# Kernel optimization log

Measured on AMD Instinct MI355X. Metric: run time of the kernel, lower is better.

The kernel has to match this reference:

```python
import jax, jax.numpy as jnp
import numpy as np

N, E, D, B, C = 50000, 800000, 128, 20000, 40
EPS_BN = 1e-3    # keras BatchNormalization default epsilon
EPS_NRM = 1e-12  # keras ops.nn.normalize epsilon
FFN_DIMS = {"pre": (D, D), "c1p": (D, D), "c1u": (2 * D, D), "c2p": (D, D), "c2u": (2 * D, D), "post": (D, D)}


def setup_inputs() -> dict:
    key = jax.random.key(0)
    ks = jax.random.split(key, 8)
    inp = {
        "node_features": jax.random.normal(ks[0], (N, D), jnp.float32),
        "edges": jax.random.randint(ks[1], (2, E), 0, N, dtype=jnp.int32),
        "edge_w": jax.random.uniform(ks[2], (E,), jnp.float32),
        "input_node_idx": jax.random.randint(ks[3], (B,), 0, N, dtype=jnp.int32),
    }
    for i, (name, (din, dout)) in enumerate(FFN_DIMS.items()):
        kw = jax.random.fold_in(key, 100 + i)
        inp[name + "_g"] = jnp.ones((din,), jnp.float32)
        inp[name + "_be"] = jnp.zeros((din,), jnp.float32)
        inp[name + "_mu"] = jnp.zeros((din,), jnp.float32)
        inp[name + "_var"] = jnp.ones((din,), jnp.float32)
        inp[name + "_w"] = jax.random.normal(kw, (din, dout), jnp.float32) * (1.0 / float(np.sqrt(din)))
        inp[name + "_bi"] = jnp.zeros((dout,), jnp.float32)
    inp["logits_w"] = jax.random.normal(ks[4], (D, C), jnp.float32) * (1.0 / float(np.sqrt(D)))
    inp["logits_b"] = jnp.zeros((C,), jnp.float32)
    return inp


def ffn(x, g, be, mu, var, w, bi):
    # BatchNorm (inference running stats) -> Dropout (identity) -> Dense + exact gelu
    xn = (x - mu) * jax.lax.rsqrt(var + EPS_BN) * g + be
    return jax.nn.gelu(xn @ w + bi, approximate=False)


def l2norm(x):
    n = jnp.sqrt(jnp.sum(x * x, axis=-1, keepdims=True))
    return x / jnp.maximum(n, EPS_NRM)


def graph_conv(x, node_idx, nbr_idx, ew, prep, upd):
    # gather neighbours -> prepare FFN -> edge-weighted -> segment_sum (reduce='sum')
    msgs = ffn(x[nbr_idx], *prep) * ew[:, None]                         # [E, D]
    red = jax.ops.segment_sum(msgs, node_idx, num_segments=x.shape[0])  # [N, D]
    h = jnp.concatenate([x, red], axis=1)                               # [N, 2D] (combination='concat')
    return l2norm(ffn(h, *upd))                                         # normalize=True


def reference(node_features, edges, edge_w, input_node_idx,
              pre_g, pre_be, pre_mu, pre_var, pre_w, pre_bi,
              c1p_g, c1p_be, c1p_mu, c1p_var, c1p_w, c1p_bi,
              c1u_g, c1u_be, c1u_mu, c1u_var, c1u_w, c1u_bi,
              c2p_g, c2p_be, c2p_mu, c2p_var, c2p_w, c2p_bi,
              c2u_g, c2u_be, c2u_mu, c2u_var, c2u_w, c2u_bi,
              post_g, post_be, post_mu, post_var, post_w, post_bi,
              logits_w, logits_b):
    ew = edge_w / jnp.sum(edge_w)                       # edge_W normalized at init
    node_idx, nbr_idx = edges[0], edges[1]
    x = ffn(node_features, pre_g, pre_be, pre_mu, pre_var, pre_w, pre_bi)
    x = graph_conv(x, node_idx, nbr_idx, ew,
                   (c1p_g, c1p_be, c1p_mu, c1p_var, c1p_w, c1p_bi),
                   (c1u_g, c1u_be, c1u_mu, c1u_var, c1u_w, c1u_bi)) + x
    x = graph_conv(x, node_idx, nbr_idx, ew,
                   (c2p_g, c2p_be, c2p_mu, c2p_var, c2p_w, c2p_bi),
                   (c2u_g, c2u_be, c2u_mu, c2u_var, c2u_w, c2u_bi)) + x
    x = ffn(x, post_g, post_be, post_mu, post_var, post_w, post_bi)
    return x[input_node_idx] @ logits_w + logits_b      # [B, C]
```

## Files before the change

kernel.cpp:

```cpp
#include <hip/hip_runtime.h>
#include <hip/hip_fp16.h>
#include <math.h>

static constexpr int D = 128;
static constexpr int CAP = 64;
static constexpr float EPS_BN = 1e-3f;

typedef short short8 __attribute__((ext_vector_type(8)));
typedef short short4v __attribute__((ext_vector_type(4)));
typedef float float4v __attribute__((ext_vector_type(4)));

__device__ __forceinline__ float gelu_exact(float x) {
    return 0.5f * x * (1.0f + erff(x * 0.70710678118654752f));
}

__device__ __forceinline__ void f32_to_hilo(float f, short& h, short& l) {
    unsigned u = __float_as_uint(f);
    h = (short)(u >> 16);
    float hf = __uint_as_float(u & 0xFFFF0000u);
    unsigned lu = __float_as_uint(f - hf);
    l = (short)(lu >> 16);
}

__device__ __forceinline__ short f32_to_bf16_rne(float f) {
    unsigned u = __float_as_uint(f);
    u += 0x7FFFu + ((u >> 16) & 1u);
    return (short)(u >> 16);
}

__device__ __forceinline__ void cvt_hilo8(const float4& x, const float4& y, short8& h8, short8& l8) {
    short h, l;
    f32_to_hilo(x.x, h, l); h8[0] = h; l8[0] = l;
    f32_to_hilo(x.y, h, l); h8[1] = h; l8[1] = l;
    f32_to_hilo(x.z, h, l); h8[2] = h; l8[2] = l;
    f32_to_hilo(x.w, h, l); h8[3] = h; l8[3] = l;
    f32_to_hilo(y.x, h, l); h8[4] = h; l8[4] = l;
    f32_to_hilo(y.y, h, l); h8[5] = h; l8[5] = l;
    f32_to_hilo(y.z, h, l); h8[6] = h; l8[6] = l;
    f32_to_hilo(y.w, h, l); h8[7] = h; l8[7] = l;
}

__device__ __forceinline__ short8 cvt_rne8(const float4& x, const float4& y) {
    short8 r;
    r[0] = f32_to_bf16_rne(x.x); r[1] = f32_to_bf16_rne(x.y);
    r[2] = f32_to_bf16_rne(x.z); r[3] = f32_to_bf16_rne(x.w);
    r[4] = f32_to_bf16_rne(y.x); r[5] = f32_to_bf16_rne(y.y);
    r[6] = f32_to_bf16_rne(y.z); r[7] = f32_to_bf16_rne(y.w);
    return r;
}

struct FoldArgs {
    const float* g[6]; const float* be[6]; const float* mu[6];
    const float* var[6]; const float* w[6]; const float* bi[6];
    short* wh[6]; short* wl[6]; float* bp[6]; int K[6];
};

__global__ void k_fold(FoldArgs fa) {
    __shared__ float sm[4];
    const int tid = threadIdx.x;
    const int lane = tid & 63, wvi = tid >> 6;
    const int f = blockIdx.x >> 7;
    const int c = blockIdx.x & 127;
    const int K = fa.K[f];
    const float* g = fa.g[f]; const float* be = fa.be[f];
    const float* mu = fa.mu[f]; const float* var = fa.var[f];
    const float* w = fa.w[f]; const float* bi = fa.bi[f];
    short* wh = fa.wh[f]; short* wl = fa.wl[f]; float* bp = fa.bp[f];
    float part = 0.f;
    for (int k = tid; k < K; k += blockDim.x) {
        float a = g[k] / sqrtf(var[k] + EPS_BN);
        float wv = w[k * D + c];
        float prod = a * wv;
        short hh, ll;
        f32_to_hilo(prod, hh, ll);
        wh[c * K + k] = hh;
        wl[c * K + k] = ll;
        part += (be[k] - mu[k] * a) * wv;
    }
    for (int off = 32; off > 0; off >>= 1) part += __shfl_down(part, off, 64);
    if (lane == 0) sm[wvi] = part;
    __syncthreads();
    if (tid == 0) bp[c] = bi[c] + sm[0] + sm[1] + sm[2] + sm[3];
}

__global__ void __launch_bounds__(512, 4) k_fillpre(
    const int* __restrict__ edges, const float* __restrict__ ew,
    int* __restrict__ cnt, float* __restrict__ sums, unsigned* __restrict__ cw,
    int E, int N,
    const float* __restrict__ A0, const short* __restrict__ Wh,
    const short* __restrict__ Wl, const float* __restrict__ bp,
    float* __restrict__ outf,
    const short* __restrict__ Wh1, const float* __restrict__ bp1,
    __half* __restrict__ yh)
{
    constexpr int K = 128;
    constexpr int WSZ = 128 * K;
    __shared__ short Wlds[2 * WSZ];
    __shared__ short xbuf[2][16][136];
    __shared__ float sm[8];

    const int tid = threadIdx.x;
    const int lane = tid & 63;
    const int wvi = tid >> 6;

    const int grp = blockIdx.x >> 8;
    const int role = grp & 1;
    const int rid = ((grp >> 1) << 8) | (blockIdx.x & 255);

    if (role == 0) {
        const int g = rid & 7;
        const int bid = rid >> 3;
        const int gs = 64 * 512;
        const int N8 = (N + 7) >> 3;
        const int lo = g * N8;
        const int hi = min(lo + N8, N);
        float s = 0.f;
        int e = bid * 512 + tid;
        for (; e + 3 * gs < E; e += 4 * gs) {
            int d0 = edges[e];
            int d1 = edges[e + gs];
            int d2 = edges[e + 2 * gs];
            int d3 = edges[e + 3 * gs];
            bool i0 = (d0 >= lo && d0 < hi);
            bool i1 = (d1 >= lo && d1 < hi);
            bool i2 = (d2 >= lo && d2 < hi);
            bool i3 = (d3 >= lo && d3 < hi);
            int s0 = 0, s1 = 0, s2 = 0, s3 = 0;
            float w0 = 0.f, w1 = 0.f, w2 = 0.f, w3 = 0.f;
            if (i0) { s0 = edges[E + e];          w0 = ew[e]; }
            if (i1) { s1 = edges[E + e + gs];     w1 = ew[e + gs]; }
            if (i2) { s2 = edges[E + e + 2 * gs]; w2 = ew[e + 2 * gs]; }
            if (i3) { s3 = edges[E + e + 3 * gs]; w3 = ew[e + 3 * gs]; }
            if (i0) { s += w0; int x = atomicAdd(&cnt[d0], 1);
                if (x < CAP) cw[(size_t)d0 * CAP + x] = ((unsigned)s0 << 16) | (unsigned)__half_as_ushort(__float2half(w0)); }
            if (i1) { s += w1; int x = atomicAdd(&cnt[d1], 1);
                if (x < CAP) cw[(size_t)d1 * CAP + x] = ((unsigned)s1 << 16) | (unsigned)__half_as_ushort(__float2half(w1)); }
            if (i2) { s += w2; int x = atomicAdd(&cnt[d2], 1);
                if (x < CAP) cw[(size_t)d2 * CAP + x] = ((unsigned)s2 << 16) | (unsigned)__half_as_ushort(__float2half(w2)); }
            if (i3) { s += w3; int x = atomicAdd(&cnt[d3], 1);
                if (x < CAP) cw[(size_t)d3 * CAP + x] = ((unsigned)s3 << 16) | (unsigned)__half_as_ushort(__float2half(w3)); }
        }
        for (; e < E; e += gs) {
            int d = edges[e];
            if (d >= lo && d < hi) {
                int src = edges[E + e];
                float w = ew[e];
                s += w;
                int x = atomicAdd(&cnt[d], 1);
                if (x < CAP)
                    cw[(size_t)d * CAP + x] = ((unsigned)src << 16) | (unsigned)__half_as_ushort(__float2half(w));
            }
        }
        for (int off = 32; off > 0; off >>= 1) s += __shfl_down(s, off, 64);
        if (lane == 0) sm[wvi] = s;
        __syncthreads();
        if (tid == 0) {
            float t = 0.f;
            #pragma unroll
            for (int i = 0; i < 8; i++) t += sm[i];
            if (t != 0.f) atomicAdd(sums, t);
        }
        return;
    }

    const int fbid = rid;
    constexpr int NBLK = 512;

    #pragma unroll
    for (int it = 0; it < (2 * WSZ) / (512 * 8); ++it) {
        int s = it * 4096 + tid * 8;
        int buf = s / WSZ;
        int rem = s - buf * WSZ;
        int c = rem / K;
        int kk = (rem & (K - 1)) ^ ((c & 7) << 3);
        const short* src = (buf ? Wl : Wh) + c * K + kk;
        *(short8*)&Wlds[s] = *(const short8*)src;
    }
    __syncthreads();

    const int wv = tid >> 6;
    const int ssub = wv >> 2;
    const int wc = wv & 3;
    const int m = lane & 15;
    const int quad = lane >> 4;
    const int nstrips = (N + 15) >> 4;
    constexpr int STRIDE = NBLK * 2;

    short8 w1f[2][2][2];
    #pragma unroll
    for (int cc = 0; cc < 2; ++cc)
        #pragma unroll
        for (int ks = 0; ks < 2; ++ks)
            #pragma unroll
            for (int tj = 0; tj < 2; ++tj) {
                const int kk = cc * 64 + ks * 32 + quad * 8;
                const int c = wc * 32 + tj * 16 + m;
                w1f[cc][ks][tj] = *(const short8*)(Wh1 + (size_t)c * 128 + kk);
            }

    int remw = nstrips - fbid * 2;
    int nit = remw > 0 ? (remw + STRIDE - 1) / STRIDE : 0;

    for (int it = 0; it < nit; ++it) {
        const int strip = fbid * 2 + ssub + it * STRIDE;
        const bool active = strip < nstrips;
        float4v acc[2];
        acc[0] = (float4v){0.f, 0.f, 0.f, 0.f};
        acc[1] = (float4v){0.f, 0.f, 0.f, 0.f};

        if (active) {
            int r = strip * 16 + m;
            if (r >= N) r = N - 1;
            const float* pA0 = A0 + (size_t)r * D;

            float4 a[2][4];
            {
                const float4* s4 = (const float4*)pA0 + quad * 2;
                a[0][0] = s4[0]; a[0][1] = s4[1]; a[0][2] = s4[8]; a[0][3] = s4[9];
            }
            {
                const float4* s4 = (const float4*)(pA0 + 64) + quad * 2;
                a[1][0] = s4[0]; a[1][1] = s4[1]; a[1][2] = s4[8]; a[1][3] = s4[9];
            }

            #pragma unroll
            for (int cc = 0; cc < 2; ++cc) {
                #pragma unroll
                for (int ks = 0; ks < 2; ++ks) {
                    const int kk = cc * 64 + ks * 32 + quad * 8;
                    short8 ah, al;
                    cvt_hilo8(a[cc][ks * 2], a[cc][ks * 2 + 1], ah, al);
                    #pragma unroll
                    for (int tj = 0; tj < 2; ++tj) {
                        const int c = wc * 32 + tj * 16 + m;
                        const int idx = c * K + (kk ^ ((c & 7) << 3));
                        short8 bh = *(const short8*)&Wlds[idx];
                        short8 bl = *(const short8*)&Wlds[WSZ + idx];
                        acc[tj] = __builtin_amdgcn_mfma_f32_16x16x32_bf16(al, bh, acc[tj], 0, 0, 0);
                        acc[tj] = __builtin_amdgcn_mfma_f32_16x16x32_bf16(ah, bl, acc[tj], 0, 0, 0);
                        acc[tj] = __builtin_amdgcn_mfma_f32_16x16x32_bf16(ah, bh, acc[tj], 0, 0, 0);
                    }
                }
            }

            #pragma unroll
            for (int tj = 0; tj < 2; ++tj) {
                float bv = bp[wc * 32 + tj * 16 + m];
                #pragma unroll
                for (int r4 = 0; r4 < 4; ++r4)
                    acc[tj][r4] = gelu_exact(acc[tj][r4] + bv);
            }
            #pragma unroll
            for (int r4 = 0; r4 < 4; ++r4) {
                int rib = quad * 4 + r4;
                int row = strip * 16 + rib;
                #pragma unroll
                for (int tj = 0; tj < 2; ++tj) {
                    int col = wc * 32 + tj * 16 + m;
                    if (row < N) outf[(size_t)row * D + col] = acc[tj][r4];
                    xbuf[ssub][rib][col] = f32_to_bf16_rne(acc[tj][r4]);
                }
            }
        }
        __syncthreads();

        if (active) {
            float4v acc2[2];
            acc2[0] = (float4v){0.f, 0.f, 0.f, 0.f};
            acc2[1] = (float4v){0.f, 0.f, 0.f, 0.f};
            #pragma unroll
            for (int cc = 0; cc < 2; ++cc) {
                #pragma unroll
                for (int ks = 0; ks < 2; ++ks) {
                    const int kk = cc * 64 + ks * 32 + quad * 8;
                    short8 ah = *(const short8*)&xbuf[ssub][m][kk];
                    #pragma unroll
                    for (int tj = 0; tj < 2; ++tj)
                        acc2[tj] = __builtin_amdgcn_mfma_f32_16x16x32_bf16(ah, w1f[cc][ks][tj], acc2[tj], 0, 0, 0);
                }
            }
            #pragma unroll
            for (int tj = 0; tj < 2; ++tj) {
                float bv = bp1[wc * 32 + tj * 16 + m];
                #pragma unroll
                for (int r4 = 0; r4 < 4; ++r4)
                    acc2[tj][r4] = gelu_exact(acc2[tj][r4] + bv);
            }
            #pragma unroll
            for (int r4 = 0; r4 < 4; ++r4) {
                int row = strip * 16 + quad * 4 + r4;
                if (row < N) {
                    #pragma unroll
                    for (int tj = 0; tj < 2; ++tj) {
                        int col = wc * 32 + tj * 16 + m;
                        yh[(size_t)row * D + col] = __float2half(acc2[tj][r4]);
                    }
                }
            }
        }
        __syncthreads();
    }
}

__device__ __forceinline__ void accum8(float* acc, const float4& raw, float w) {
    const __half2* hp = (const __half2*)&raw;
    #pragma unroll
    for (int t = 0; t < 4; t++) {
        float2 f = __half22float2(hp[t]);
        acc[t * 2]     += w * f.x;
        acc[t * 2 + 1] += w * f.y;
    }
}

__global__ void k_reduce(const int* __restrict__ cnt, const unsigned* __restrict__ cw,
                         const float* __restrict__ sums, const __half* __restrict__ y,
                         float* __restrict__ red, int N) {
    int n = blockIdx.x * (blockDim.x >> 6) + (threadIdx.x >> 6);
    if (n >= N) return;
    float inv = 1.0f / sums[0];
    int lane = threadIdx.x & 63;
    int sub = lane >> 4;
    int q = lane & 15;
    int count = min(cnt[n], CAP);
    int start = n * CAP;
    int end = start + count;
    float acc[8] = {0.f, 0.f, 0.f, 0.f, 0.f, 0.f, 0.f, 0.f};
    int i = start + sub;
    for (; i + 12 < end; i += 16) {
        unsigned c0 = cw[i];
        unsigned c1 = cw[i + 4];
        unsigned c2 = cw[i + 8];
        unsigned c3 = cw[i + 12];
        float4 r0 = *((const float4*)(y + (size_t)(c0 >> 16) * D) + q);
        float4 r1 = *((const float4*)(y + (size_t)(c1 >> 16) * D) + q);
        float4 r2 = *((const float4*)(y + (size_t)(c2 >> 16) * D) + q);
        float4 r3 = *((const float4*)(y + (size_t)(c3 >> 16) * D) + q);
        float w0 = __half2float(__ushort_as_half((unsigned short)(c0 & 0xFFFFu))) * inv;
        float w1 = __half2float(__ushort_as_half((unsigned short)(c1 & 0xFFFFu))) * inv;
        float w2 = __half2float(__ushort_as_half((unsigned short)(c2 & 0xFFFFu))) * inv;
        float w3 = __half2float(__ushort_as_half((unsigned short)(c3 & 0xFFFFu))) * inv;
        accum8(acc, r0, w0);
        accum8(acc, r1, w1);
        accum8(acc, r2, w2);
        accum8(acc, r3, w3);
    }
    for (; i < end; i += 4) {
        unsigned c = cw[i];
        float4 r = *((const float4*)(y + (size_t)(c >> 16) * D) + q);
        float w = __half2float(__ushort_as_half((unsigned short)(c & 0xFFFFu))) * inv;
        accum8(acc, r, w);
    }
    #pragma unroll
    for (int t = 0; t < 8; t++) {
        acc[t] += __shfl_xor(acc[t], 16, 64);
        acc[t] += __shfl_xor(acc[t], 32, 64);
    }
    if (sub == 0) {
        float4 o0 = {acc[0], acc[1], acc[2], acc[3]};
        float4 o1 = {acc[4], acc[5], acc[6], acc[7]};
        *((float4*)(red + (size_t)n * D + q * 8)) = o0;
        *((float4*)(red + (size_t)n * D + q * 8 + 4)) = o1;
    }
}

template<int K, int BLOCK, bool SPLIT3, bool L2RES, bool OUT16, bool GATHER, bool FUSEP>
__global__ void __launch_bounds__(BLOCK, BLOCK / 256) k_ffn(
    const float* __restrict__ A0, const float* __restrict__ A1,
    const short* __restrict__ Wh, const short* __restrict__ Wl,
    const float* __restrict__ bp, const float* __restrict__ resid,
    float* __restrict__ outf, __half* __restrict__ outh, int N,
    const int* __restrict__ gidx,
    const short* __restrict__ WhP, const float* __restrict__ bpP,
    __half* __restrict__ yhP)
{
    constexpr int NB = SPLIT3 ? 2 : 1;
    constexpr int WSZ = 128 * K;
    constexpr int NC = K / 64;
    constexpr int SS = BLOCK / 256;
    __shared__ short Wlds[NB * WSZ];
    __shared__ float rsum[SS][16][4];
    __shared__ short xbuf[FUSEP ? SS : 1][16][136];

    const int tid = threadIdx.x;

    constexpr int ITER = (NB * WSZ) / (BLOCK * 8);
    #pragma unroll
    for (int it = 0; it < ITER; ++it) {
        int s = it * (BLOCK * 8) + tid * 8;
        int buf = s / WSZ;
        int rem = s - buf * WSZ;
        int c = rem / K;
        int kk = (rem & (K - 1)) ^ ((c & 7) << 3);
        const short* src = (buf ? Wl : Wh) + c * K + kk;
        *(short8*)&Wlds[s] = *(const short8*)src;
    }
    __syncthreads();

    const int lane = tid & 63;
    const int wv = tid >> 6;
    const int ssub = wv >> 2;
    const int wc = wv & 3;
    const int m = lane & 15;
    const int quad = lane >> 4;
    const int nstrips = (N + 15) >> 4;
    const int stride = gridDim.x * SS;
    const int base = blockIdx.x * SS + ssub;

    auto body = [&](int strip, bool active) {
        int rr = active ? strip * 16 + m : m;
        if (rr >= N) rr = N - 1;
        const int r = GATHER ? gidx[rr] : rr;
        const float* pA0 = A0 + (size_t)r * D;
        const float* pA1 = (K == 256) ? (A1 + (size_t)r * D) : pA0;

        float4 a[2][4];
        {
            const float4* s4 = (const float4*)pA0 + quad * 2;
            a[0][0] = s4[0]; a[0][1] = s4[1]; a[0][2] = s4[8]; a[0][3] = s4[9];
        }
        {
            const float4* s4 = (const float4*)(pA0 + 64) + quad * 2;
            a[1][0] = s4[0]; a[1][1] = s4[1]; a[1][2] = s4[8]; a[1][3] = s4[9];
        }

        float4v acc[2];
        acc[0] = (float4v){0.f, 0.f, 0.f, 0.f};
        acc[1] = (float4v){0.f, 0.f, 0.f, 0.f};

        #pragma unroll
        for (int cc = 0; cc < NC; ++cc) {
            #pragma unroll
            for (int ks = 0; ks < 2; ++ks) {
                const int kk = cc * 64 + ks * 32 + quad * 8;
                short8 ah, al;
                if (SPLIT3) cvt_hilo8(a[cc & 1][ks * 2], a[cc & 1][ks * 2 + 1], ah, al);
                else        ah = cvt_rne8(a[cc & 1][ks * 2], a[cc & 1][ks * 2 + 1]);
                #pragma unroll
                for (int tj = 0; tj < 2; ++tj) {
                    const int c = wc * 32 + tj * 16 + m;
                    const int idx = c * K + (kk ^ ((c & 7) << 3));
                    short8 bh = *(const short8*)&Wlds[idx];
                    if (SPLIT3) {
                        short8 bl = *(const short8*)&Wlds[WSZ + idx];
                        acc[tj] = __builtin_amdgcn_mfma_f32_16x16x32_bf16(al, bh, acc[tj], 0, 0, 0);
                        acc[tj] = __builtin_amdgcn_mfma_f32_16x16x32_bf16(ah, bl, acc[tj], 0, 0, 0);
                    }
                    acc[tj] = __builtin_amdgcn_mfma_f32_16x16x32_bf16(ah, bh, acc[tj], 0, 0, 0);
                }
            }
            if (cc + 2 < NC) {
                const int n2 = cc + 2;
                const float* src = (K == 256 && n2 >= 2) ? pA1 : pA0;
                const int kb = (K == 256) ? ((n2 & 1) * 64) : (n2 * 64);
                const float4* s4 = (const float4*)(src + kb) + quad * 2;
                a[cc & 1][0] = s4[0]; a[cc & 1][1] = s4[1];
                a[cc & 1][2] = s4[8]; a[cc & 1][3] = s4[9];
            }
        }

        #pragma unroll
        for (int tj = 0; tj < 2; ++tj) {
            float bv = bp[wc * 32 + tj * 16 + m];
            #pragma unroll
            for (int r4 = 0; r4 < 4; ++r4)
                acc[tj][r4] = gelu_exact(acc[tj][r4] + bv);
        }

        if (L2RES) {
            float ss[4];
            #pragma unroll
            for (int r4 = 0; r4 < 4; ++r4) {
                float v = acc[0][r4] * acc[0][r4] + acc[1][r4] * acc[1][r4];
                v += __shfl_xor(v, 1, 64);
                v += __shfl_xor(v, 2, 64);
                v += __shfl_xor(v, 4, 64);
                v += __shfl_xor(v, 8, 64);
                ss[r4] = v;
            }
            if (m == 0) {
                #pragma unroll
                for (int r4 = 0; r4 < 4; ++r4) rsum[ssub][quad * 4 + r4][wc] = ss[r4];
            }
            __syncthreads();
            #pragma unroll
            for (int r4 = 0; r4 < 4; ++r4) {
                const int rib = quad * 4 + r4;
                float tot = rsum[ssub][rib][0] + rsum[ssub][rib][1]
                          + rsum[ssub][rib][2] + rsum[ssub][rib][3];
                float inv = 1.0f / fmaxf(sqrtf(tot), 1e-12f);
                int row = strip * 16 + rib;
                if (active && row < N) {
                    #pragma unroll
                    for (int tj = 0; tj < 2; ++tj) {
                        int col = wc * 32 + tj * 16 + m;
                        float v = acc[tj][r4] * inv + resid[(size_t)row * D + col];
                        outf[(size_t)row * D + col] = v;
                        if (FUSEP) xbuf[ssub][rib][col] = f32_to_bf16_rne(v);
                    }
                }
            }
            if (FUSEP) {
                __syncthreads();
                if (active) {
                    float4v acc2[2];
                    acc2[0] = (float4v){0.f, 0.f, 0.f, 0.f};
                    acc2[1] = (float4v){0.f, 0.f, 0.f, 0.f};
                    #pragma unroll
                    for (int cc = 0; cc < 2; ++cc) {
                        #pragma unroll
                        for (int ks = 0; ks < 2; ++ks) {
                            const int kk = cc * 64 + ks * 32 + quad * 8;
                            short8 ah = *(const short8*)&xbuf[ssub][m][kk];
                            #pragma unroll
                            for (int tj = 0; tj < 2; ++tj) {
                                const int c = wc * 32 + tj * 16 + m;
                                short8 bh = *(const short8*)(WhP + (size_t)c * 128 + kk);
                                acc2[tj] = __builtin_amdgcn_mfma_f32_16x16x32_bf16(ah, bh, acc2[tj], 0, 0, 0);
                            }
                        }
                    }
                    #pragma unroll
                    for (int tj = 0; tj < 2; ++tj) {
                        float bv = bpP[wc * 32 + tj * 16 + m];
                        #pragma unroll
                        for (int r4 = 0; r4 < 4; ++r4)
                            acc2[tj][r4] = gelu_exact(acc2[tj][r4] + bv);
                    }
                    #pragma unroll
                    for (int r4 = 0; r4 < 4; ++r4) {
                        int row = strip * 16 + quad * 4 + r4;
                        if (row < N) {
                            #pragma unroll
                            for (int tj = 0; tj < 2; ++tj) {
                                int col = wc * 32 + tj * 16 + m;
                                yhP[(size_t)row * D + col] = __float2half(acc2[tj][r4]);
                            }
                        }
                    }
                }
            }
            __syncthreads();
        } else {
            #pragma unroll
            for (int r4 = 0; r4 < 4; ++r4) {
                int row = strip * 16 + quad * 4 + r4;
                if (active && row < N) {
                    #pragma unroll
                    for (int tj = 0; tj < 2; ++tj) {
                        int col = wc * 32 + tj * 16 + m;
                        if (OUT16) outh[(size_t)row * D + col] = __float2half(acc[tj][r4]);
                        else       outf[(size_t)row * D + col] = acc[tj][r4];
                    }
                }
            }
        }
    };

    if (L2RES) {
        int rem = nstrips - blockIdx.x * SS;
        int nit = rem > 0 ? (rem + stride - 1) / stride : 0;
        for (int it = 0; it < nit; ++it) {
            int strip = base + it * stride;
            body(strip, strip < nstrips);
        }
    } else {
        for (int strip = base; strip < nstrips; strip += stride)
            body(strip, true);
    }
}

__global__ void k_logits(const float* __restrict__ x,
                         const float* __restrict__ LW, const float* __restrict__ lb,
                         float* __restrict__ out, int B) {
    int wid = blockIdx.x * 4 + (threadIdx.x >> 6);
    int lane = threadIdx.x & 63;
    if (wid >= B) return;
    if (lane >= 40) return;
    float acc = lb[lane];
    const float4* xr = (const float4*)(x + (size_t)wid * D);
    #pragma unroll 4
    for (int k4 = 0; k4 < 32; k4++) {
        float4 xv = xr[k4];
        acc += xv.x * LW[(4 * k4 + 0) * 40 + lane];
        acc += xv.y * LW[(4 * k4 + 1) * 40 + lane];
        acc += xv.z * LW[(4 * k4 + 2) * 40 + lane];
        acc += xv.w * LW[(4 * k4 + 3) * 40 + lane];
    }
    out[(size_t)wid * 40 + lane] = acc;
}

extern "C" void kernel_launch(void* const* d_in, const int* in_sizes, int n_in,
                              void* d_out, int out_size, void* d_ws, size_t ws_size,
                              hipStream_t stream) {
    const float* node_features = (const float*)d_in[0];
    const int*   edges         = (const int*)d_in[1];
    const float* edge_w        = (const float*)d_in[2];
    const int*   input_idx     = (const int*)d_in[3];
    const int N = in_sizes[0] / D;
    const int E = in_sizes[2];
    const int B = in_sizes[3];

    const float* P[6][6];
    for (int f = 0; f < 6; f++)
        for (int q = 0; q < 6; q++)
            P[f][q] = (const float*)d_in[4 + f * 6 + q];
    const float* logits_w = (const float*)d_in[40];
    const float* logits_b = (const float*)d_in[41];

    float* ws = (float*)d_ws;
    size_t nd = (size_t)N * D;
    float* xA  = ws;
    float* y   = ws + nd;
    float* red = ws + 2 * nd;
    float* p   = ws + 3 * nd;
    __half* yh = (__half*)p; p += nd / 2;
    const int Ks[6] = {128, 128, 256, 128, 256, 128};
    short* Wh[6]; short* Wl[6]; float* Bp[6];
    {
        short* sp = (short*)p;
        for (int f = 0; f < 6; f++) {
            Wh[f] = sp; sp += (size_t)Ks[f] * D;
            Wl[f] = sp; sp += (size_t)Ks[f] * D;
        }
        p = (float*)sp;
    }
    for (int f = 0; f < 6; f++) { Bp[f] = p; p += D; }
    int* cnt    = (int*)p; p += N;
    float* sums = p; p += 2;
    unsigned* cw = (unsigned*)p; p += (size_t)N * CAP;

    FoldArgs fa;
    for (int f = 0; f < 6; f++) {
        fa.g[f] = P[f][0]; fa.be[f] = P[f][1]; fa.mu[f] = P[f][2];
        fa.var[f] = P[f][3]; fa.w[f] = P[f][4]; fa.bi[f] = P[f][5];
        fa.wh[f] = Wh[f]; fa.wl[f] = Wl[f]; fa.bp[f] = Bp[f]; fa.K[f] = Ks[f];
    }

    hipMemsetAsync(cnt, 0, ((size_t)N + 2) * sizeof(int), stream);
    k_fold<<<768, 256, 0, stream>>>(fa);
    k_fillpre<<<1024, 512, 0, stream>>>(edges, edge_w, cnt, sums, cw, E, N,
                                        node_features, Wh[0], Wl[0], Bp[0], xA,
                                        Wh[1], Bp[1], yh);

    const int rb = (N + 3) / 4;
    const int g1 = 256;
    const int g2 = 512;

    k_reduce<<<rb, 256, 0, stream>>>(cnt, cw, sums, yh, red, N);
    k_ffn<256, 1024, true,  true,  false, false, true ><<<g1, 1024, 0, stream>>>(
        xA, red, Wh[2], Wl[2], Bp[2], xA, y, nullptr, N, nullptr, Wh[3], Bp[3], yh);
    k_reduce<<<rb, 256, 0, stream>>>(cnt, cw, sums, yh, red, N);
    k_ffn<256, 1024, true,  true,  false, false, false><<<g1, 1024, 0, stream>>>(
        y, red, Wh[4], Wl[4], Bp[4], y, xA, nullptr, N, nullptr, nullptr, nullptr, nullptr);
    k_ffn<128, 512,  true,  false, false, true,  false><<<g2, 512, 0, stream>>>(
        xA, nullptr, Wh[5], Wl[5], Bp[5], nullptr, red, nullptr, B, input_idx, nullptr, nullptr, nullptr);
    k_logits<<<(B + 3) / 4, 256, 0, stream>>>(red, logits_w, logits_b, (float*)d_out, B);
}
```

Measured before the change: 434.7 us.

## Overlap neighbour reduction with the x-half of the update GEMM

Replaces the standalone reduce kernel with a dual-role kernel. Half of the blocks do the edge gather/segment-sum, while the other half compute the x-half of the concat update GEMM (K=128 slice of the 256-wide weights) and store fp32 partial sums. The update FFN then runs with K=128 over the reduced features only, seeding its accumulators from those partials. The aim is to run the memory-bound gather concurrently with MFMA work. The cost is an extra full-size fp32 partial buffer written and read back through existing y/xA storage.

New measurement: 453.3 us. 4.3% more time.

```diff
diff --git a/kernel.cpp b/kernel.cpp
--- a/kernel.cpp
+++ b/kernel.cpp
@@ -7,7 +7,6 @@
 static constexpr float EPS_BN = 1e-3f;
 
 typedef short short8 __attribute__((ext_vector_type(8)));
-typedef short short4v __attribute__((ext_vector_type(4)));
 typedef float float4v __attribute__((ext_vector_type(4)));
 
 __device__ __forceinline__ float gelu_exact(float x) {
@@ -38,15 +37,6 @@
     f32_to_hilo(y.y, h, l); h8[5] = h; l8[5] = l;
     f32_to_hilo(y.z, h, l); h8[6] = h; l8[6] = l;
     f32_to_hilo(y.w, h, l); h8[7] = h; l8[7] = l;
-}
-
-__device__ __forceinline__ short8 cvt_rne8(const float4& x, const float4& y) {
-    short8 r;
-    r[0] = f32_to_bf16_rne(x.x); r[1] = f32_to_bf16_rne(x.y);
-    r[2] = f32_to_bf16_rne(x.z); r[3] = f32_to_bf16_rne(x.w);
-    r[4] = f32_to_bf16_rne(y.x); r[5] = f32_to_bf16_rne(y.y);
-    r[6] = f32_to_bf16_rne(y.z); r[7] = f32_to_bf16_rne(y.w);
-    return r;
 }
 
 struct FoldArgs {
@@ -302,68 +292,163 @@
     }
 }
 
-__device__ __forceinline__ void accum8(float* acc, const float4& raw, float w) {
-    const __half2* hp = (const __half2*)&raw;
+__global__ void __launch_bounds__(512, 4) k_redgemm(
+    const int* __restrict__ cnt, const unsigned* __restrict__ cw,
+    const float* __restrict__ sums, const __half* __restrict__ yh,
+    float* __restrict__ red, int N,
+    const float* __restrict__ A0, const short* __restrict__ Whh,
+    const short* __restrict__ Wlh,
+    float* __restrict__ pacc)
+{
+    constexpr int K = 128;
+    constexpr int WSZ = 128 * K;
+    __shared__ short Wlds[2 * WSZ];
+
+    const int tid = threadIdx.x;
+    const int lane = tid & 63;
+    const int wv = tid >> 6;
+
+    const int grp = blockIdx.x >> 8;
+    const int role = grp & 1;
+    const int rid = ((grp >> 1) << 8) | (blockIdx.x & 255);
+
+    if (role == 0) {
+        float inv = 1.0f / sums[0];
+        const int sub = lane >> 4;
+        const int q = lane & 15;
+        for (int n = rid * 8 + wv; n < N; n += 4096) {
+            int count = min(cnt[n], CAP);
+            int start = n * CAP;
+            int end = start + count;
+            float acc[8] = {0.f, 0.f, 0.f, 0.f, 0.f, 0.f, 0.f, 0.f};
+            int i = start + sub;
+            for (; i + 12 < end; i += 16) {
+                unsigned c0 = cw[i];
+                unsigned c1 = cw[i + 4];
+                unsigned c2 = cw[i + 8];
+                unsigned c3 = cw[i + 12];
+                float4 r0 = *((const float4*)(yh + (size_t)(c0 >> 16) * D) + q);
+                float4 r1 = *((const float4*)(yh + (size_t)(c1 >> 16) * D) + q);
+                float4 r2 = *((const float4*)(yh + (size_t)(c2 >> 16) * D) + q);
+                float4 r3 = *((const float4*)(yh + (size_t)(c3 >> 16) * D) + q);
+                float w0 = __half2float(__ushort_as_half((unsigned short)(c0 & 0xFFFFu))) * inv;
+                float w1 = __half2float(__ushort_as_half((unsigned short)(c1 & 0xFFFFu))) * inv;
+                float w2 = __half2float(__ushort_as_half((unsigned short)(c2 & 0xFFFFu))) * inv;
+                float w3 = __half2float(__ushort_as_half((unsigned short)(c3 & 0xFFFFu))) * inv;
+                const __half2* h0 = (const __half2*)&r0;
+                const __half2* h1 = (const __half2*)&r1;
+                const __half2* h2 = (const __half2*)&r2;
+                const __half2* h3 = (const __half2*)&r3;
+                #pragma unroll
+                for (int t = 0; t < 4; t++) {
+                    float2 f0 = __half22float2(h0[t]);
+                    float2 f1 = __half22float2(h1[t]);
+                    float2 f2 = __half22float2(h2[t]);
+                    float2 f3 = __half22float2(h3[t]);
+                    acc[t*2]   += w0 * f0.x; acc[t*2+1] += w0 * f0.y;
+                    acc[t*2]   += w1 * f1.x; acc[t*2+1] += w1 * f1.y;
+                    acc[t*2]   += w2 * f2.x; acc[t*2+1] += w2 * f2.y;
+                    acc[t*2]   += w3 * f3.x; acc[t*2+1] += w3 * f3.y;
+                }
+            }
+            for (; i < end; i += 4) {
+                unsigned c = cw[i];
+                float4 r = *((const float4*)(yh + (size_t)(c >> 16) * D) + q);
+                float w = __half2float(__ushort_as_half((unsigned short)(c & 0xFFFFu))) * inv;
+                const __half2* hp = (const __half2*)&r;
+                #pragma unroll
+                for (int t = 0; t < 4; t++) {
+                    float2 f = __half22float2(hp[t]);
+                    acc[t*2]   += w * f.x;
+                    acc[t*2+1] += w * f.y;
+                }
+            }
+            #pragma unroll
+            for (int t = 0; t < 8; t++) {
+                acc[t] += __shfl_xor(acc[t], 16, 64);
+                acc[t] += __shfl_xor(acc[t], 32, 64);
+            }
+            if (sub == 0) {
+                float4 o0 = {acc[0], acc[1], acc[2], acc[3]};
+                float4 o1 = {acc[4], acc[5], acc[6], acc[7]};
+                *((float4*)(red + (size_t)n * D + q * 8)) = o0;
+                *((float4*)(red + (size_t)n * D + q * 8 + 4)) = o1;
+            }
+        }
+        return;
+    }
+
     #pragma unroll
-    for (int t = 0; t < 4; t++) {
-        float2 f = __half22float2(hp[t]);
-        acc[t * 2]     += w * f.x;
-        acc[t * 2 + 1] += w * f.y;
-    }
-}
-
-__global__ void k_reduce(const int* __restrict__ cnt, const unsigned* __restrict__ cw,
-                         const float* __restrict__ sums, const __half* __restrict__ y,
-                         float* __restrict__ red, int N) {
-    int n = blockIdx.x * (blockDim.x >> 6) + (threadIdx.x >> 6);
-    if (n >= N) return;
-    float inv = 1.0f / sums[0];
-    int lane = threadIdx.x & 63;
-    int sub = lane >> 4;
-    int q = lane & 15;
-    int count = min(cnt[n], CAP);
-    int start = n * CAP;
-    int end = start + count;
-    float acc[8] = {0.f, 0.f, 0.f, 0.f, 0.f, 0.f, 0.f, 0.f};
-    int i = start + sub;
-    for (; i + 12 < end; i += 16) {
-        unsigned c0 = cw[i];
-        unsigned c1 = cw[i + 4];
-        unsigned c2 = cw[i + 8];
-        unsigned c3 = cw[i + 12];
-        float4 r0 = *((const float4*)(y + (size_t)(c0 >> 16) * D) + q);
-        float4 r1 = *((const float4*)(y + (size_t)(c1 >> 16) * D) + q);
-        float4 r2 = *((const float4*)(y + (size_t)(c2 >> 16) * D) + q);
-        float4 r3 = *((const float4*)(y + (size_t)(c3 >> 16) * D) + q);
-        float w0 = __half2float(__ushort_as_half((unsigned short)(c0 & 0xFFFFu))) * inv;
-        float w1 = __half2float(__ushort_as_half((unsigned short)(c1 & 0xFFFFu))) * inv;
-        float w2 = __half2float(__ushort_as_half((unsigned short)(c2 & 0xFFFFu))) * inv;
-        float w3 = __half2float(__ushort_as_half((unsigned short)(c3 & 0xFFFFu))) * inv;
-        accum8(acc, r0, w0);
-        accum8(acc, r1, w1);
-        accum8(acc, r2, w2);
-        accum8(acc, r3, w3);
-    }
-    for (; i < end; i += 4) {
-        unsigned c = cw[i];
-        float4 r = *((const float4*)(y + (size_t)(c >> 16) * D) + q);
-        float w = __half2float(__ushort_as_half((unsigned short)(c & 0xFFFFu))) * inv;
-        accum8(acc, r, w);
-    }
-    #pragma unroll
-    for (int t = 0; t < 8; t++) {
-        acc[t] += __shfl_xor(acc[t], 16, 64);
-        acc[t] += __shfl_xor(acc[t], 32, 64);
-    }
-    if (sub == 0) {
-        float4 o0 = {acc[0], acc[1], acc[2], acc[3]};
-        float4 o1 = {acc[4], acc[5], acc[6], acc[7]};
-        *((float4*)(red + (size_t)n * D + q * 8)) = o0;
-        *((float4*)(red + (size_t)n * D + q * 8 + 4)) = o1;
-    }
-}
-
-template<int K, int BLOCK, bool SPLIT3, bool L2RES, bool OUT16, bool GATHER, bool FUSEP>
+    for (int it = 0; it < (2 * WSZ) / (512 * 8); ++it) {
+        int s = it * 4096 + tid * 8;
+        int buf = s / WSZ;
+        int rem = s - buf * WSZ;
+        int c = rem / K;
+        int kk = (rem & (K - 1)) ^ ((c & 7) << 3);
+        const short* src = (buf ? Wlh : Whh) + (size_t)c * 256 + kk;
+        *(short8*)&Wlds[s] = *(const short8*)src;
+    }
+    __syncthreads();
+
+    const int ssub = wv >> 2;
+    const int wc = wv & 3;
+    const int m = lane & 15;
+    const int quad = lane >> 4;
+    const int nstrips = (N + 15) >> 4;
+
+    for (int strip = rid * 2 + ssub; strip < nstrips; strip += 1024) {
+        int r = strip * 16 + m;
+        if (r >= N) r = N - 1;
+        const float* pA0 = A0 + (size_t)r * D;
+
+        float4 a[2][4];
+        {
+            const float4* s4 = (const float4*)pA0 + quad * 2;
+            a[0][0] = s4[0]; a[0][1] = s4[1]; a[0][2] = s4[8]; a[0][3] = s4[9];
+        }
+        {
+            const float4* s4 = (const float4*)(pA0 + 64) + quad * 2;
+            a[1][0] = s4[0]; a[1][1] = s4[1]; a[1][2] = s4[8]; a[1][3] = s4[9];
+        }
+
+        float4v acc[2];
+        acc[0] = (float4v){0.f, 0.f, 0.f, 0.f};
+        acc[1] = (float4v){0.f, 0.f, 0.f, 0.f};
+
+        #pragma unroll
+        for (int cc = 0; cc < 2; ++cc) {
+            #pragma unroll
+            for (int ks = 0; ks < 2; ++ks) {
+                const int kk = cc * 64 + ks * 32 + quad * 8;
+                short8 ah, al;
+                cvt_hilo8(a[cc][ks * 2], a[cc][ks * 2 + 1], ah, al);
+                #pragma unroll
+                for (int tj = 0; tj < 2; ++tj) {
+                    const int c = wc * 32 + tj * 16 + m;
+                    const int idx = c * K + (kk ^ ((c & 7) << 3));
+                    short8 bh = *(const short8*)&Wlds[idx];
+                    short8 bl = *(const short8*)&Wlds[WSZ + idx];
+                    acc[tj] = __builtin_amdgcn_mfma_f32_16x16x32_bf16(al, bh, acc[tj], 0, 0, 0);
+                    acc[tj] = __builtin_amdgcn_mfma_f32_16x16x32_bf16(ah, bl, acc[tj], 0, 0, 0);
+                    acc[tj] = __builtin_amdgcn_mfma_f32_16x16x32_bf16(ah, bh, acc[tj], 0, 0, 0);
+                }
+            }
+        }
+        #pragma unroll
+        for (int r4 = 0; r4 < 4; ++r4) {
+            int row = strip * 16 + quad * 4 + r4;
+            if (row < N) {
+                #pragma unroll
+                for (int tj = 0; tj < 2; ++tj) {
+                    int col = wc * 32 + tj * 16 + m;
+                    pacc[(size_t)row * D + col] = acc[tj][r4];
+                }
+            }
+        }
+    }
+}
+
+template<int K, int BLOCK, int KS, bool SPLIT3, bool L2RES, bool OUT16, bool GATHER, bool FUSEP, bool PACCIN>
 __global__ void __launch_bounds__(BLOCK, BLOCK / 256) k_ffn(
     const float* __restrict__ A0, const float* __restrict__ A1,
     const short* __restrict__ Wh, const short* __restrict__ Wl,
@@ -371,7 +456,8 @@
     float* __restrict__ outf, __half* __restrict__ outh, int N,
     const int* __restrict__ gidx,
     const short* __restrict__ WhP, const float* __restrict__ bpP,
-    __half* __restrict__ yhP)
+    __half* __restrict__ yhP,
+    const float* __restrict__ pacc)
 {
     constexpr int NB = SPLIT3 ? 2 : 1;
     constexpr int WSZ = 128 * K;
@@ -391,7 +477,7 @@
         int rem = s - buf * WSZ;
         int c = rem / K;
         int kk = (rem & (K - 1)) ^ ((c & 7) << 3);
-        const short* src = (buf ? Wl : Wh) + c * K + kk;
+        const short* src = (buf ? Wl : Wh) + (size_t)c * KS + kk;
         *(short8*)&Wlds[s] = *(const short8*)src;
     }
     __syncthreads();
@@ -424,8 +510,19 @@
         }
 
         float4v acc[2];
-        acc[0] = (float4v){0.f, 0.f, 0.f, 0.f};
-        acc[1] = (float4v){0.f, 0.f, 0.f, 0.f};
+        if (PACCIN) {
+            #pragma unroll
+            for (int tj = 0; tj < 2; ++tj)
+                #pragma unroll
+                for (int r4 = 0; r4 < 4; ++r4) {
+                    int row = strip * 16 + quad * 4 + r4;
+                    int rowc = row < N ? row : N - 1;
+                    acc[tj][r4] = pacc[(size_t)rowc * D + wc * 32 + tj * 16 + m];
+                }
+        } else {
+            acc[0] = (float4v){0.f, 0.f, 0.f, 0.f};
+            acc[1] = (float4v){0.f, 0.f, 0.f, 0.f};
+        }
 
         #pragma unroll
         for (int cc = 0; cc < NC; ++cc) {
@@ -434,7 +531,13 @@
                 const int kk = cc * 64 + ks * 32 + quad * 8;
                 short8 ah, al;
                 if (SPLIT3) cvt_hilo8(a[cc & 1][ks * 2], a[cc & 1][ks * 2 + 1], ah, al);
-                else        ah = cvt_rne8(a[cc & 1][ks * 2], a[cc & 1][ks * 2 + 1]);
+                else {
+                    float4 x = a[cc & 1][ks * 2], y = a[cc & 1][ks * 2 + 1];
+                    ah[0] = f32_to_bf16_rne(x.x); ah[1] = f32_to_bf16_rne(x.y);
+                    ah[2] = f32_to_bf16_rne(x.z); ah[3] = f32_to_bf16_rne(x.w);
+                    ah[4] = f32_to_bf16_rne(y.x); ah[5] = f32_to_bf16_rne(y.y);
+                    ah[6] = f32_to_bf16_rne(y.z); ah[7] = f32_to_bf16_rne(y.w);
+                }
                 #pragma unroll
                 for (int tj = 0; tj < 2; ++tj) {
                     const int c = wc * 32 + tj * 16 + m;
@@ -642,17 +745,19 @@
                                         node_features, Wh[0], Wl[0], Bp[0], xA,
                                         Wh[1], Bp[1], yh);
 
-    const int rb = (N + 3) / 4;
     const int g1 = 256;
     const int g2 = 512;
 
-    k_reduce<<<rb, 256, 0, stream>>>(cnt, cw, sums, yh, red, N);
-    k_ffn<256, 1024, true,  true,  false, false, true ><<<g1, 1024, 0, stream>>>(
-        xA, red, Wh[2], Wl[2], Bp[2], xA, y, nullptr, N, nullptr, Wh[3], Bp[3], yh);
-    k_reduce<<<rb, 256, 0, stream>>>(cnt, cw, sums, yh, red, N);
-    k_ffn<256, 1024, true,  true,  false, false, false><<<g1, 1024, 0, stream>>>(
-        y, red, Wh[4], Wl[4], Bp[4], y, xA, nullptr, N, nullptr, nullptr, nullptr, nullptr);
-    k_ffn<128, 512,  true,  false, false, true,  false><<<g2, 512, 0, stream>>>(
-        xA, nullptr, Wh[5], Wl[5], Bp[5], nullptr, red, nullptr, B, input_idx, nullptr, nullptr, nullptr);
+    k_redgemm<<<1024, 512, 0, stream>>>(cnt, cw, sums, yh, red, N, xA, Wh[2], Wl[2], y);
+    k_ffn<128, 1024, 256, true, true, false, false, true, true><<<g1, 1024, 0, stream>>>(
+        red, nullptr, Wh[2] + 128, Wl[2] + 128, Bp[2], xA, y, nullptr, N, nullptr,
+        Wh[3], Bp[3], yh, y);
+    k_redgemm<<<1024, 512, 0, stream>>>(cnt, cw, sums, yh, red, N, y, Wh[4], Wl[4], xA);
+    k_ffn<128, 1024, 256, true, true, false, false, false, true><<<g1, 1024, 0, stream>>>(
+        red, nullptr, Wh[4] + 128, Wl[4] + 128, Bp[4], y, xA, nullptr, N, nullptr,
+        nullptr, nullptr, nullptr, xA);
+    k_ffn<128, 512, 128, true, false, false, true, false, false><<<g2, 512, 0, stream>>>(
+        xA, nullptr, Wh[5], Wl[5], Bp[5], nullptr, red, nullptr, B, input_idx,
+        nullptr, nullptr, nullptr, nullptr);
     k_logits<<<(B + 3) / 4, 256, 0, stream>>>(red, logits_w, logits_b, (float*)d_out, B);
 }
```
